# Kernel tuning notes

Measured on AMD Instinct MI355X. Metric: run time of the kernel, lower is better.

The kernel has to match this reference:

```python
import jax, jax.numpy as jnp
import numpy as np

NUM_CLASSES = 19
K = 100                 # max_views_per_class
TEMP = 0.1
BASE_TEMP = 0.07
EPS_NORM = 1e-12


def _l2_normalize(x):
    # matches torch F.normalize(dim=1): x / max(||x||, eps)
    n = jnp.sqrt(jnp.sum(x * x, axis=1, keepdims=True))
    return x / jnp.maximum(n, EPS_NORM)


def _sample_indices(labels_flat):
    # Deterministic per-class sampler: first K pixels of each class.
    # (torch version uses randperm; the downstream math is identical.)
    # Every class is guaranteed >= K pixels by input construction.
    idxs = [jnp.where(labels_flat == c, size=K, fill_value=0)[0]
            for c in range(NUM_CLASSES)]
    return jnp.concatenate(idxs)  # [NUM_CLASSES*K]


def setup_inputs() -> dict:
    key = jax.random.key(0)
    k1, k2, k3, k4 = jax.random.split(key, 4)
    pixel_feats = jax.random.normal(k1, (8, 256, 128, 128), dtype=jnp.float32)
    labels = jax.random.randint(k2, (8, 128, 128), 0, NUM_CLASSES).astype(jnp.int64)
    memory_feats = jax.random.normal(k3, (20000, 256), dtype=jnp.float32)
    memory_labels = jax.random.randint(k4, (20000,), 0, NUM_CLASSES).astype(jnp.int64)
    return {"pixel_feats": pixel_feats, "labels": labels,
            "memory_feats": memory_feats, "memory_labels": memory_labels}


def reference(pixel_feats, labels, memory_feats, memory_labels):
    B, D, H, W = pixel_feats.shape
    feats_flat = pixel_feats.transpose(0, 2, 3, 1).reshape(-1, D)   # [B*H*W, D]
    labels_flat = labels.reshape(-1)

    idx = _sample_indices(labels_flat)
    anchor_feats = feats_flat[idx]                                  # [Na, D]
    anchor_labels = jnp.repeat(jnp.arange(NUM_CLASSES), K)          # [Na]

    contrast_feats = jnp.concatenate([anchor_feats, memory_feats], axis=0)
    contrast_labels = jnp.concatenate([anchor_labels, memory_labels], axis=0)

    a = _l2_normalize(anchor_feats)
    c = _l2_normalize(contrast_feats)
    logits = jnp.einsum('nd,md->nm', a, c) / TEMP                   # [Na, Nc]

    Na, Nc = logits.shape
    mask = (anchor_labels[:, None] == contrast_labels[None, :]).astype(logits.dtype)
    # remove self-contrast (diagonal of the first Na contrast columns)
    rows = jnp.arange(Na)
    logits_mask = jnp.ones((Na, Nc), dtype=logits.dtype).at[rows, rows].set(0.0)
    mask = mask * logits_mask

    exp_logits = jnp.exp(logits) * logits_mask
    log_prob = logits - jnp.log(exp_logits.sum(axis=1, keepdims=True) + 1e-12)

    pos_count = mask.sum(axis=1)                                    # [Na]
    valid = pos_count > 0
    mean_log_prob_pos = (mask * log_prob).sum(axis=1) / jnp.maximum(pos_count, 1.0)
    n_valid = jnp.maximum(jnp.sum(valid).astype(logits.dtype), 1.0)
    loss = -(TEMP / BASE_TEMP) * (jnp.sum(jnp.where(valid, mean_log_prob_pos, 0.0)) / n_valid)
    return loss
```

## Files before the change

### kernel.cpp

```cpp
#include <hip/hip_runtime.h>
#include <hip/hip_bf16.h>
#include <math.h>

#define NCLS   19
#define KPC    100
#define NA     1900
#define NM     20000
#define NC     21900
#define NCP2   22016
#define D      256
#define HW     16384
#define NPIX   131072
#define NT_M   15
#define NT_N   172

typedef __attribute__((ext_vector_type(8))) short bf16x8;
typedef __attribute__((ext_vector_type(4))) float f32x4;

#define WS_IDX   0
#define WS_ROWS  7680
#define WS_ROWP  15360
#define WS_ROWC  23040
#define WS_CLAB  30720
#define WS_CT2   118784

__device__ __forceinline__ short f2bf(float x) {
    __hip_bfloat16 h = __float2bfloat16(x);
    return *(short*)&h;
}

__global__ void init_kernel(float* rowS, float* rowP, float* rowC, int* clab,
                            const int* __restrict__ memlab, short* __restrict__ Ct2) {
    const int i = blockIdx.x * 256 + threadIdx.x;
    if (i < NCP2) clab[i] = (i < NA) ? ((i * 5243) >> 19)
                                     : ((i < NC) ? memlab[i - NA] : -1);
    if (i < 1920) { rowS[i] = 0.f; rowP[i] = 0.f; rowC[i] = 0.f; }
    if (i < 32 * (NCP2 - NC)) {
        const int kq = i / (NCP2 - NC);
        const int n  = NC + i % (NCP2 - NC);
        bf16x8 z = {};
        *(bf16x8*)(Ct2 + ((size_t)kq * NCP2 + n) * 8) = z;
    }
}

__global__ void sample_kernel(const int* __restrict__ labels, int* __restrict__ idx) {
    const int c = blockIdx.x;
    const int t = threadIdx.x;
    const int wave = t >> 6, lane = t & 63;
    __shared__ int s_base;
    __shared__ int s_wavecnt[4];
    if (t == 0) s_base = 0;
    __syncthreads();
    for (int start = 0; start < NPIX; start += 256) {
        const int i = start + t;
        const bool pred = (labels[i] == c);
        const unsigned long long b = __ballot(pred);
        if (lane == 0) s_wavecnt[wave] = __popcll(b);
        __syncthreads();
        const int base = s_base;
        int wbase = 0;
        for (int w = 0; w < wave; ++w) wbase += s_wavecnt[w];
        const int chunk_total = s_wavecnt[0] + s_wavecnt[1] + s_wavecnt[2] + s_wavecnt[3];
        if (pred) {
            const int rank = base + wbase + __popcll(b & ((1ULL << lane) - 1ULL));
            if (rank < KPC) idx[c * KPC + rank] = i;
        }
        __syncthreads();
        if (t == 0) s_base = base + chunk_total;
        if (base + chunk_total >= KPC) break;
    }
}

__global__ void anchor_kernel(const float* __restrict__ pixel, const int* __restrict__ idx,
                              short* __restrict__ Ct2) {
    const int t = threadIdx.x;
    const int a = blockIdx.x * 8 + (t >> 5);
    const int kq = t & 31;
    if (a >= NA) return;
    const int p = idx[a];
    const int b = p >> 14;
    const int hw = p & (HW - 1);
    const float* base = pixel + ((size_t)(b * D + kq * 8)) * HW + hw;
    float v[8];
    float ssq = 0.f;
    #pragma unroll
    for (int j = 0; j < 8; ++j) { v[j] = base[(size_t)j * HW]; ssq += v[j] * v[j]; }
    #pragma unroll
    for (int o = 16; o; o >>= 1) ssq += __shfl_xor(ssq, o, 32);
    const float inv = 1.0f / fmaxf(sqrtf(ssq), 1e-12f);
    bf16x8 out;
    #pragma unroll
    for (int j = 0; j < 8; ++j) out[j] = f2bf(v[j] * inv);
    *(bf16x8*)(Ct2 + ((size_t)kq * NCP2 + a) * 8) = out;
}

__global__ void memory_kernel(const float* __restrict__ mem, short* __restrict__ Ct2) {
    const int t = threadIdx.x;
    const int r = blockIdx.x * 8 + (t >> 5);
    const int kq = t & 31;
    const float4 v0 = *(const float4*)(mem + (size_t)r * D + kq * 8);
    const float4 v1 = *(const float4*)(mem + (size_t)r * D + kq * 8 + 4);
    float ssq = v0.x*v0.x + v0.y*v0.y + v0.z*v0.z + v0.w*v0.w
              + v1.x*v1.x + v1.y*v1.y + v1.z*v1.z + v1.w*v1.w;
    #pragma unroll
    for (int o = 16; o; o >>= 1) ssq += __shfl_xor(ssq, o, 32);
    const float inv = 1.0f / fmaxf(sqrtf(ssq), 1e-12f);
    bf16x8 out;
    out[0] = f2bf(v0.x * inv); out[1] = f2bf(v0.y * inv);
    out[2] = f2bf(v0.z * inv); out[3] = f2bf(v0.w * inv);
    out[4] = f2bf(v1.x * inv); out[5] = f2bf(v1.y * inv);
    out[6] = f2bf(v1.z * inv); out[7] = f2bf(v1.w * inv);
    *(bf16x8*)(Ct2 + ((size_t)kq * NCP2 + NA + r) * 8) = out;
}

__global__ __launch_bounds__(256, 3)
void mfma_gemm_kernel(const short* __restrict__ Ct2, const int* __restrict__ clab,
                      float* __restrict__ rowS, float* __restrict__ rowP,
                      float* __restrict__ rowC) {
    __shared__ __align__(16) short As[8 * 128 * 8];
    __shared__ __align__(16) short Bs[8 * 128 * 8];
    const int tid  = threadIdx.x;
    const int lane = tid & 63;
    const int w    = tid >> 6;
    const int wm   = w >> 1, wn = w & 1;
    const int m0   = blockIdx.x * 128;
    const int n0   = blockIdx.y * 128;
    const int quad = lane >> 4;
    const int l16  = lane & 15;

    f32x4 acc[4][4] = {};

    for (int kc = 0; kc < 4; ++kc) {
        #pragma unroll
        for (int i = 0; i < 4; ++i) {
            const int bl = (w * 4 + i) * 64;
            const int kq = bl >> 7;
            const int ml = bl & 127;
            const size_t gA = ((size_t)(kc * 8 + kq) * NCP2 + m0 + ml + lane) * 8;
            __builtin_amdgcn_global_load_lds(
                (const __attribute__((address_space(1))) void*)(Ct2 + gA),
                (__attribute__((address_space(3))) void*)(As + (size_t)bl * 8 + lane * 8),
                16, 0, 0);
            const size_t gB = ((size_t)(kc * 8 + kq) * NCP2 + n0 + ml + lane) * 8;
            __builtin_amdgcn_global_load_lds(
                (const __attribute__((address_space(1))) void*)(Ct2 + gB),
                (__attribute__((address_space(3))) void*)(Bs + (size_t)bl * 8 + lane * 8),
                16, 0, 0);
        }
        __syncthreads();
        #pragma unroll
        for (int ks = 0; ks < 2; ++ks) {
            const int kqb = ks * 4 + quad;
            bf16x8 af[4], bfr[4];
            #pragma unroll
            for (int mi = 0; mi < 4; ++mi)
                af[mi] = *(const bf16x8*)(As + ((kqb * 128) + wm * 64 + mi * 16 + l16) * 8);
            #pragma unroll
            for (int ni = 0; ni < 4; ++ni)
                bfr[ni] = *(const bf16x8*)(Bs + ((kqb * 128) + wn * 64 + ni * 16 + l16) * 8);
            #pragma unroll
            for (int mi = 0; mi < 4; ++mi)
                #pragma unroll
                for (int ni = 0; ni < 4; ++ni)
                    acc[mi][ni] = __builtin_amdgcn_mfma_f32_16x16x32_bf16(
                        af[mi], bfr[ni], acc[mi][ni], 0, 0, 0);
        }
        __syncthreads();
    }

    int nIdx[4], nLab[4];
    #pragma unroll
    for (int ni = 0; ni < 4; ++ni) {
        const int n = n0 + wn * 64 + ni * 16 + l16;
        nIdx[ni] = n;
        nLab[ni] = (n < NC) ? clab[n] : -1;
    }
    #pragma unroll
    for (int mi = 0; mi < 4; ++mi) {
        #pragma unroll
        for (int r = 0; r < 4; ++r) {
            const int m = m0 + wm * 64 + mi * 16 + quad * 4 + r;
            const int mlab = (m * 5243) >> 19;
            float s = 0.f, p = 0.f, cnt = 0.f;
            #pragma unroll
            for (int ni = 0; ni < 4; ++ni) {
                const int n = nIdx[ni];
                if (n < NC && n != m) {
                    const float l = acc[mi][ni][r] * 10.0f;
                    s += __expf(l);
                    if (nLab[ni] == mlab) { p += l; cnt += 1.f; }
                }
            }
            for (int o = 1; o < 16; o <<= 1) {
                s   += __shfl_xor(s, o, 64);
                p   += __shfl_xor(p, o, 64);
                cnt += __shfl_xor(cnt, o, 64);
            }
            if (l16 == 0 && m < NA) {
                atomicAdd(&rowS[m], s);
                atomicAdd(&rowP[m], p);
                atomicAdd(&rowC[m], cnt);
            }
        }
    }
}

__global__ void finalize_kernel(const float* __restrict__ rowS, const float* __restrict__ rowP,
                                const float* __restrict__ rowC, float* __restrict__ out) {
    const int t = threadIdx.x;
    float sum = 0.f, nval = 0.f;
    for (int n = t; n < NA; n += 256) {
        const float cnt = rowC[n];
        const float logS = logf(rowS[n] + 1e-12f);
        const float mean = (rowP[n] - cnt * logS) / fmaxf(cnt, 1.0f);
        if (cnt > 0.f) { sum += mean; nval += 1.f; }
    }
    for (int o = 32; o; o >>= 1) {
        sum += __shfl_xor(sum, o, 64);
        nval += __shfl_xor(nval, o, 64);
    }
    __shared__ float rs[4], rn[4];
    if ((t & 63) == 0) { rs[t >> 6] = sum; rn[t >> 6] = nval; }
    __syncthreads();
    if (t == 0) {
        const float s = rs[0] + rs[1] + rs[2] + rs[3];
        const float nv = rn[0] + rn[1] + rn[2] + rn[3];
        out[0] = -(0.1f / 0.07f) * (s / fmaxf(nv, 1.f));
    }
}

extern "C" void kernel_launch(void* const* d_in, const int* in_sizes, int n_in,
                              void* d_out, int out_size, void* d_ws, size_t ws_size,
                              hipStream_t stream) {
    const float* pixel  = (const float*)d_in[0];
    const int*   labels = (const int*)d_in[1];
    const float* mem    = (const float*)d_in[2];
    const int*   memlab = (const int*)d_in[3];
    char* ws = (char*)d_ws;
    int*   idx  = (int*)(ws + WS_IDX);
    float* rowS = (float*)(ws + WS_ROWS);
    float* rowP = (float*)(ws + WS_ROWP);
    float* rowC = (float*)(ws + WS_ROWC);
    int*   clab = (int*)(ws + WS_CLAB);
    short* Ct2  = (short*)(ws + WS_CT2);
    float* out  = (float*)d_out;

    init_kernel<<<dim3(86), dim3(256), 0, stream>>>(rowS, rowP, rowC, clab, memlab, Ct2);
    sample_kernel<<<dim3(NCLS), dim3(256), 0, stream>>>(labels, idx);
    anchor_kernel<<<dim3(238), dim3(256), 0, stream>>>(pixel, idx, Ct2);
    memory_kernel<<<dim3(2500), dim3(256), 0, stream>>>(mem, Ct2);
    mfma_gemm_kernel<<<dim3(NT_M, NT_N), dim3(256), 0, stream>>>(Ct2, clab, rowS, rowP, rowC);
    finalize_kernel<<<dim3(1), dim3(256), 0, stream>>>(rowS, rowP, rowC, out);
}
```

Baseline: 263.3 us.

## Keep A tile resident in LDS, stream double-buffered B tiles, fuse finalize

The GEMM now loads each 128-row anchor tile with the full K dimension into LDS once. Each block then loops over several contrast tiles, streaming B chunks through a double buffer and reducing the epilogue per tile. The finalize step moves into the GEMM's last block via an atomic ticket, and the memory normalization and init kernels merge into one prep kernel. Positive counts come from a label histogram instead of per-element atomics. The grid is smaller with lower occupancy, and the count formula assumes every class is present.

```diff
diff --git a/kernel.cpp b/kernel.cpp
--- a/kernel.cpp
+++ b/kernel.cpp
@@ -12,7 +12,7 @@
 #define HW     16384
 #define NPIX   131072
 #define NT_M   15
-#define NT_N   172
+#define NGRP   34
 
 typedef __attribute__((ext_vector_type(8))) short bf16x8;
 typedef __attribute__((ext_vector_type(4))) float f32x4;
@@ -20,26 +20,55 @@
 #define WS_IDX   0
 #define WS_ROWS  7680
 #define WS_ROWP  15360
-#define WS_ROWC  23040
-#define WS_CLAB  30720
-#define WS_CT2   118784
+#define WS_HIST  23040
+#define WS_TKT   23168
+#define WS_CLAB  23296
+#define WS_CT2   111616
 
 __device__ __forceinline__ short f2bf(float x) {
     __hip_bfloat16 h = __float2bfloat16(x);
     return *(short*)&h;
 }
 
-__global__ void init_kernel(float* rowS, float* rowP, float* rowC, int* clab,
-                            const int* __restrict__ memlab, short* __restrict__ Ct2) {
-    const int i = blockIdx.x * 256 + threadIdx.x;
-    if (i < NCP2) clab[i] = (i < NA) ? ((i * 5243) >> 19)
-                                     : ((i < NC) ? memlab[i - NA] : -1);
-    if (i < 1920) { rowS[i] = 0.f; rowP[i] = 0.f; rowC[i] = 0.f; }
-    if (i < 32 * (NCP2 - NC)) {
-        const int kq = i / (NCP2 - NC);
-        const int n  = NC + i % (NCP2 - NC);
-        bf16x8 z = {};
-        *(bf16x8*)(Ct2 + ((size_t)kq * NCP2 + n) * 8) = z;
+__global__ void prep_kernel(const float* __restrict__ mem, const int* __restrict__ memlab,
+                            float* rowS, float* rowP, int* clab, int* hist, int* ticket,
+                            short* __restrict__ Ct2) {
+    const int b = blockIdx.x, t = threadIdx.x;
+    if (b < 2500) {
+        const int r = b * 8 + (t >> 5);
+        const int kq = t & 31;
+        const float4 v0 = *(const float4*)(mem + (size_t)r * D + kq * 8);
+        const float4 v1 = *(const float4*)(mem + (size_t)r * D + kq * 8 + 4);
+        float ssq = v0.x*v0.x + v0.y*v0.y + v0.z*v0.z + v0.w*v0.w
+                  + v1.x*v1.x + v1.y*v1.y + v1.z*v1.z + v1.w*v1.w;
+        #pragma unroll
+        for (int o = 16; o; o >>= 1) ssq += __shfl_xor(ssq, o, 32);
+        const float inv = 1.0f / fmaxf(sqrtf(ssq), 1e-12f);
+        bf16x8 outv;
+        outv[0] = f2bf(v0.x * inv); outv[1] = f2bf(v0.y * inv);
+        outv[2] = f2bf(v0.z * inv); outv[3] = f2bf(v0.w * inv);
+        outv[4] = f2bf(v1.x * inv); outv[5] = f2bf(v1.y * inv);
+        outv[6] = f2bf(v1.z * inv); outv[7] = f2bf(v1.w * inv);
+        *(bf16x8*)(Ct2 + ((size_t)kq * NCP2 + NA + r) * 8) = outv;
+    } else if (b < 2586) {
+        const int i = (b - 2500) * 256 + t;
+        clab[i] = (i < NA) ? ((i * 5243) >> 19)
+                           : ((i < NC) ? memlab[i - NA] : -1);
+        if (i < 1920) { rowS[i] = 0.f; rowP[i] = 0.f; }
+        if (i < 32 * (NCP2 - NC)) {
+            const int kq = i / (NCP2 - NC);
+            const int n  = NC + (i - kq * (NCP2 - NC));
+            bf16x8 z = {};
+            *(bf16x8*)(Ct2 + ((size_t)kq * NCP2 + n) * 8) = z;
+        }
+    } else {
+        __shared__ int h[NCLS];
+        if (t < NCLS) h[t] = 0;
+        if (t == 32) *ticket = 0;
+        __syncthreads();
+        for (int i = t; i < NM; i += 256) atomicAdd(&h[memlab[i]], 1);
+        __syncthreads();
+        if (t < NCLS) hist[t] = h[t];
     }
 }
 
@@ -88,144 +117,148 @@
     #pragma unroll
     for (int o = 16; o; o >>= 1) ssq += __shfl_xor(ssq, o, 32);
     const float inv = 1.0f / fmaxf(sqrtf(ssq), 1e-12f);
-    bf16x8 out;
-    #pragma unroll
-    for (int j = 0; j < 8; ++j) out[j] = f2bf(v[j] * inv);
-    *(bf16x8*)(Ct2 + ((size_t)kq * NCP2 + a) * 8) = out;
-}
-
-__global__ void memory_kernel(const float* __restrict__ mem, short* __restrict__ Ct2) {
-    const int t = threadIdx.x;
-    const int r = blockIdx.x * 8 + (t >> 5);
-    const int kq = t & 31;
-    const float4 v0 = *(const float4*)(mem + (size_t)r * D + kq * 8);
-    const float4 v1 = *(const float4*)(mem + (size_t)r * D + kq * 8 + 4);
-    float ssq = v0.x*v0.x + v0.y*v0.y + v0.z*v0.z + v0.w*v0.w
-              + v1.x*v1.x + v1.y*v1.y + v1.z*v1.z + v1.w*v1.w;
-    #pragma unroll
-    for (int o = 16; o; o >>= 1) ssq += __shfl_xor(ssq, o, 32);
-    const float inv = 1.0f / fmaxf(sqrtf(ssq), 1e-12f);
-    bf16x8 out;
-    out[0] = f2bf(v0.x * inv); out[1] = f2bf(v0.y * inv);
-    out[2] = f2bf(v0.z * inv); out[3] = f2bf(v0.w * inv);
-    out[4] = f2bf(v1.x * inv); out[5] = f2bf(v1.y * inv);
-    out[6] = f2bf(v1.z * inv); out[7] = f2bf(v1.w * inv);
-    *(bf16x8*)(Ct2 + ((size_t)kq * NCP2 + NA + r) * 8) = out;
-}
-
-__global__ __launch_bounds__(256, 3)
-void mfma_gemm_kernel(const short* __restrict__ Ct2, const int* __restrict__ clab,
-                      float* __restrict__ rowS, float* __restrict__ rowP,
-                      float* __restrict__ rowC) {
-    __shared__ __align__(16) short As[8 * 128 * 8];
-    __shared__ __align__(16) short Bs[8 * 128 * 8];
+    bf16x8 outv;
+    #pragma unroll
+    for (int j = 0; j < 8; ++j) outv[j] = f2bf(v[j] * inv);
+    *(bf16x8*)(Ct2 + ((size_t)kq * NCP2 + a) * 8) = outv;
+}
+
+__global__ __launch_bounds__(256, 2)
+void gemm_kernel(const short* __restrict__ Ct2, const int* __restrict__ clab,
+                 float* __restrict__ rowS, float* __restrict__ rowP,
+                 const int* __restrict__ hist, int* ticket, float* __restrict__ out) {
+    __shared__ __align__(16) short lds[40960];
+    short* As = lds;
+    short* Bs = lds + 32768;
     const int tid  = threadIdx.x;
     const int lane = tid & 63;
     const int w    = tid >> 6;
     const int wm   = w >> 1, wn = w & 1;
-    const int m0   = blockIdx.x * 128;
-    const int n0   = blockIdx.y * 128;
     const int quad = lane >> 4;
     const int l16  = lane & 15;
-
-    f32x4 acc[4][4] = {};
-
-    for (int kc = 0; kc < 4; ++kc) {
-        #pragma unroll
-        for (int i = 0; i < 4; ++i) {
-            const int bl = (w * 4 + i) * 64;
-            const int kq = bl >> 7;
-            const int ml = bl & 127;
-            const size_t gA = ((size_t)(kc * 8 + kq) * NCP2 + m0 + ml + lane) * 8;
-            __builtin_amdgcn_global_load_lds(
-                (const __attribute__((address_space(1))) void*)(Ct2 + gA),
-                (__attribute__((address_space(3))) void*)(As + (size_t)bl * 8 + lane * 8),
-                16, 0, 0);
-            const size_t gB = ((size_t)(kc * 8 + kq) * NCP2 + n0 + ml + lane) * 8;
+    const int mt   = blockIdx.x;
+    const int g    = blockIdx.y;
+    const int m0   = mt * 128;
+    const int NTILE = (g < 2) ? 6 : 5;
+    const int NCH   = NTILE * 8;
+
+    #pragma unroll
+    for (int i = 0; i < 16; ++i) {
+        const int c  = w * 16 + i;
+        const int kq = c >> 1;
+        const int ml = (c & 1) * 64;
+        const size_t gA = ((size_t)kq * NCP2 + m0 + ml + lane) * 8;
+        __builtin_amdgcn_global_load_lds(
+            (const __attribute__((address_space(1))) void*)(Ct2 + gA),
+            (__attribute__((address_space(3))) void*)(As + ((size_t)(kq * 128 + ml)) * 8 + lane * 8),
+            16, 0, 0);
+    }
+
+    auto issueB = [&](int c, int buf) {
+        const int n0  = (g + NGRP * (c >> 3)) * 128;
+        const int kq0 = (c & 7) * 4;
+        #pragma unroll
+        for (int i = 0; i < 2; ++i) {
+            const int cc  = w * 2 + i;
+            const int kql = cc >> 1;
+            const int nl  = (cc & 1) * 64;
+            const size_t gB = ((size_t)(kq0 + kql) * NCP2 + n0 + nl + lane) * 8;
             __builtin_amdgcn_global_load_lds(
                 (const __attribute__((address_space(1))) void*)(Ct2 + gB),
-                (__attribute__((address_space(3))) void*)(Bs + (size_t)bl * 8 + lane * 8),
+                (__attribute__((address_space(3))) void*)(Bs + (size_t)buf * 4096 + (kql * 128 + nl) * 8 + lane * 8),
                 16, 0, 0);
         }
-        __syncthreads();
-        #pragma unroll
-        for (int ks = 0; ks < 2; ++ks) {
-            const int kqb = ks * 4 + quad;
-            bf16x8 af[4], bfr[4];
-            #pragma unroll
-            for (int mi = 0; mi < 4; ++mi)
-                af[mi] = *(const bf16x8*)(As + ((kqb * 128) + wm * 64 + mi * 16 + l16) * 8);
+    };
+
+    issueB(0, 0);
+    f32x4 acc[4][4] = {};
+
+    for (int c = 0; c < NCH; ++c) {
+        __syncthreads();
+        if (c + 1 < NCH) issueB(c + 1, (c + 1) & 1);
+        const short* Bb = Bs + (c & 1) * 4096;
+        const int kc = c & 7;
+        bf16x8 af[4], bfr[4];
+        #pragma unroll
+        for (int mi = 0; mi < 4; ++mi)
+            af[mi] = *(const bf16x8*)(As + ((kc * 4 + quad) * 128 + wm * 64 + mi * 16 + l16) * 8);
+        #pragma unroll
+        for (int ni = 0; ni < 4; ++ni)
+            bfr[ni] = *(const bf16x8*)(Bb + (quad * 128 + wn * 64 + ni * 16 + l16) * 8);
+        #pragma unroll
+        for (int mi = 0; mi < 4; ++mi)
             #pragma unroll
             for (int ni = 0; ni < 4; ++ni)
-                bfr[ni] = *(const bf16x8*)(Bs + ((kqb * 128) + wn * 64 + ni * 16 + l16) * 8);
+                acc[mi][ni] = __builtin_amdgcn_mfma_f32_16x16x32_bf16(
+                    af[mi], bfr[ni], acc[mi][ni], 0, 0, 0);
+
+        if (kc == 7) {
+            const int n0t = (g + NGRP * (c >> 3)) * 128;
+            int nIdx[4], nLab[4];
+            #pragma unroll
+            for (int ni = 0; ni < 4; ++ni) {
+                const int n = n0t + wn * 64 + ni * 16 + l16;
+                nIdx[ni] = n;
+                nLab[ni] = (n < NC) ? clab[n] : -1;
+            }
+            #pragma unroll
+            for (int mi = 0; mi < 4; ++mi) {
+                #pragma unroll
+                for (int r = 0; r < 4; ++r) {
+                    const int m = m0 + wm * 64 + mi * 16 + quad * 4 + r;
+                    const int mlab = (m * 5243) >> 19;
+                    float s = 0.f, p = 0.f;
+                    #pragma unroll
+                    for (int ni = 0; ni < 4; ++ni) {
+                        const int n = nIdx[ni];
+                        if (n < NC && n != m) {
+                            const float l = acc[mi][ni][r] * 10.0f;
+                            s += __expf(l);
+                            if (nLab[ni] == mlab) p += l;
+                        }
+                    }
+                    #pragma unroll
+                    for (int o = 1; o < 16; o <<= 1) {
+                        s += __shfl_xor(s, o, 64);
+                        p += __shfl_xor(p, o, 64);
+                    }
+                    if (l16 == 0 && m < NA) {
+                        atomicAdd(&rowS[m], s);
+                        atomicAdd(&rowP[m], p);
+                    }
+                }
+            }
             #pragma unroll
             for (int mi = 0; mi < 4; ++mi)
                 #pragma unroll
                 for (int ni = 0; ni < 4; ++ni)
-                    acc[mi][ni] = __builtin_amdgcn_mfma_f32_16x16x32_bf16(
-                        af[mi], bfr[ni], acc[mi][ni], 0, 0, 0);
-        }
-        __syncthreads();
-    }
-
-    int nIdx[4], nLab[4];
-    #pragma unroll
-    for (int ni = 0; ni < 4; ++ni) {
-        const int n = n0 + wn * 64 + ni * 16 + l16;
-        nIdx[ni] = n;
-        nLab[ni] = (n < NC) ? clab[n] : -1;
-    }
-    #pragma unroll
-    for (int mi = 0; mi < 4; ++mi) {
-        #pragma unroll
-        for (int r = 0; r < 4; ++r) {
-            const int m = m0 + wm * 64 + mi * 16 + quad * 4 + r;
-            const int mlab = (m * 5243) >> 19;
-            float s = 0.f, p = 0.f, cnt = 0.f;
-            #pragma unroll
-            for (int ni = 0; ni < 4; ++ni) {
-                const int n = nIdx[ni];
-                if (n < NC && n != m) {
-                    const float l = acc[mi][ni][r] * 10.0f;
-                    s += __expf(l);
-                    if (nLab[ni] == mlab) { p += l; cnt += 1.f; }
-                }
-            }
-            for (int o = 1; o < 16; o <<= 1) {
-                s   += __shfl_xor(s, o, 64);
-                p   += __shfl_xor(p, o, 64);
-                cnt += __shfl_xor(cnt, o, 64);
-            }
-            if (l16 == 0 && m < NA) {
-                atomicAdd(&rowS[m], s);
-                atomicAdd(&rowP[m], p);
-                atomicAdd(&rowC[m], cnt);
-            }
-        }
-    }
-}
-
-__global__ void finalize_kernel(const float* __restrict__ rowS, const float* __restrict__ rowP,
-                                const float* __restrict__ rowC, float* __restrict__ out) {
-    const int t = threadIdx.x;
-    float sum = 0.f, nval = 0.f;
-    for (int n = t; n < NA; n += 256) {
-        const float cnt = rowC[n];
-        const float logS = logf(rowS[n] + 1e-12f);
-        const float mean = (rowP[n] - cnt * logS) / fmaxf(cnt, 1.0f);
-        if (cnt > 0.f) { sum += mean; nval += 1.f; }
-    }
-    for (int o = 32; o; o >>= 1) {
-        sum += __shfl_xor(sum, o, 64);
-        nval += __shfl_xor(nval, o, 64);
-    }
-    __shared__ float rs[4], rn[4];
-    if ((t & 63) == 0) { rs[t >> 6] = sum; rn[t >> 6] = nval; }
+                    acc[mi][ni] = f32x4{};
+        }
+    }
+
     __syncthreads();
-    if (t == 0) {
-        const float s = rs[0] + rs[1] + rs[2] + rs[3];
-        const float nv = rn[0] + rn[1] + rn[2] + rn[3];
-        out[0] = -(0.1f / 0.07f) * (s / fmaxf(nv, 1.f));
+    int* flag = (int*)(lds + 32768);
+    if (tid == 0) {
+        __threadfence();
+        const int o = atomicAdd(ticket, 1);
+        flag[0] = (o == NT_M * NGRP - 1) ? 1 : 0;
+    }
+    __syncthreads();
+    if (flag[0]) {
+        __threadfence();
+        float sum = 0.f;
+        for (int n = tid; n < NA; n += 256) {
+            const int cls = (n * 5243) >> 19;
+            const float cnt = 99.0f + (float)hist[cls];
+            const float logS = logf(rowS[n] + 1e-12f);
+            sum += (rowP[n] - cnt * logS) / cnt;
+        }
+        #pragma unroll
+        for (int o = 32; o; o >>= 1) sum += __shfl_xor(sum, o, 64);
+        float* rs = (float*)lds;
+        if (lane == 0) rs[w] = sum;
+        __syncthreads();
+        if (tid == 0) out[0] = -(10.0f / 7.0f) * ((rs[0] + rs[1] + rs[2] + rs[3]) / 1900.0f);
     }
 }
 
@@ -240,15 +273,14 @@
     int*   idx  = (int*)(ws + WS_IDX);
     float* rowS = (float*)(ws + WS_ROWS);
     float* rowP = (float*)(ws + WS_ROWP);
-    float* rowC = (float*)(ws + WS_ROWC);
+    int*   hist = (int*)(ws + WS_HIST);
+    int*   tkt  = (int*)(ws + WS_TKT);
     int*   clab = (int*)(ws + WS_CLAB);
     short* Ct2  = (short*)(ws + WS_CT2);
     float* out  = (float*)d_out;
 
-    init_kernel<<<dim3(86), dim3(256), 0, stream>>>(rowS, rowP, rowC, clab, memlab, Ct2);
+    prep_kernel<<<dim3(2587), dim3(256), 0, stream>>>(mem, memlab, rowS, rowP, clab, hist, tkt, Ct2);
     sample_kernel<<<dim3(NCLS), dim3(256), 0, stream>>>(labels, idx);
     anchor_kernel<<<dim3(238), dim3(256), 0, stream>>>(pixel, idx, Ct2);
-    memory_kernel<<<dim3(2500), dim3(256), 0, stream>>>(mem, Ct2);
-    mfma_gemm_kernel<<<dim3(NT_M, NT_N), dim3(256), 0, stream>>>(Ct2, clab, rowS, rowP, rowC);
-    finalize_kernel<<<dim3(1), dim3(256), 0, stream>>>(rowS, rowP, rowC, out);
-}
+    gemm_kernel<<<dim3(NT_M, NGRP), dim3(256), 0, stream>>>(Ct2, clab, rowS, rowP, hist, tkt, out);
+}
```

New measurement: 303.2 us. +15.1%, slower.
